# Kernel tuning notes

Measured on AMD Instinct MI355X. Metric: run time of the kernel, lower is better.

## Reference

```python
import jax, jax.numpy as jnp
import numpy as np

N = 50000        # nodes
E = 800000       # edges (before self-loops)
IN_C = 256
OUT_C = 64
HEADS = 4
NEG_SLOPE = 0.2  # PyG GATConv default


def setup_inputs() -> dict:
    key = jax.random.key(0)
    k0, k1, k2, k3, k4 = jax.random.split(key, 5)
    x = jax.random.normal(k0, (N, IN_C), jnp.float32)
    edge_index = jax.random.randint(k1, (2, E), 0, N, dtype=jnp.int32)
    W = jax.random.normal(k2, (IN_C, HEADS * OUT_C), jnp.float32) * (1.0 / np.sqrt(IN_C))
    att_src = jax.random.normal(k3, (HEADS, OUT_C), jnp.float32) * 0.1
    att_dst = jax.random.normal(k4, (HEADS, OUT_C), jnp.float32) * 0.1
    bias = jnp.zeros((OUT_C,), jnp.float32)
    return {"x": x, "edge_index": edge_index, "W": W,
            "att_src": att_src, "att_dst": att_dst, "bias": bias}


def reference(x, edge_index, W, att_src, att_dst, bias):
    n = x.shape[0]
    # PyG GATConv default add_self_loops=True
    loop = jnp.arange(n, dtype=edge_index.dtype)
    src = jnp.concatenate([edge_index[0], loop])  # [E+N]
    dst = jnp.concatenate([edge_index[1], loop])  # [E+N]

    h = (x @ W).reshape(n, HEADS, OUT_C)                    # [N,H,C]
    a_src = jnp.einsum('nhc,hc->nh', h, att_src)            # [N,H]
    a_dst = jnp.einsum('nhc,hc->nh', h, att_dst)            # [N,H]

    e = jax.nn.leaky_relu(a_src[src] + a_dst[dst], NEG_SLOPE)   # [E',H]
    # segment softmax over edges grouped by destination node
    m = jax.lax.stop_gradient(jax.ops.segment_max(e, dst, num_segments=n))  # [N,H]
    ex = jnp.exp(e - m[dst])
    denom = jax.ops.segment_sum(ex, dst, num_segments=n)    # [N,H]
    alpha = ex / (denom[dst] + 1e-16)                       # [E',H]

    out = jax.ops.segment_sum(alpha[:, :, None] * h[src], dst, num_segments=n)  # [N,H,C]
    # concat=False -> mean over heads, then bias
    return out.mean(axis=1) + bias
```

## Files before the change

### kernel.cpp

```cpp
#include <hip/hip_runtime.h>
#include <hip/hip_bf16.h>

#define INC   256
#define HEADS 4
#define OUTC  64
#define NEG_SLOPE 0.2f
#define CAP   5120
#define EPB_A 4096

typedef __attribute__((ext_vector_type(8))) short  fragA;
typedef __attribute__((ext_vector_type(4))) float  f32x4;

__device__ __forceinline__ float bf2f(unsigned short u) {
    union { unsigned int i; float f; } v; v.i = ((unsigned int)u) << 16; return v.f;
}
__device__ __forceinline__ unsigned short f2bf(float x) {
    __hip_bfloat16 b = __float2bfloat16(x);
    return *reinterpret_cast<unsigned short*>(&b);
}

__global__ __launch_bounds__(256) void wt_zero_kernel(const float* __restrict__ W,
                                                      unsigned short* __restrict__ Wt,
                                                      int* __restrict__ btail, int nbuck)
{
    int idx = blockIdx.x * 256 + threadIdx.x;
    int k = idx >> 8, c = idx & 255;
    Wt[c * 256 + k] = f2bf(W[k * 256 + c]);
    if (idx < nbuck) btail[idx] = 0;
}

__global__ __launch_bounds__(256, 2) void gemm_passA(
    const float* __restrict__ A,
    const unsigned short* __restrict__ Wt,
    const float* __restrict__ att_src,
    const float* __restrict__ att_dst,
    unsigned short* __restrict__ H2,
    float* __restrict__ a_srcO,
    float* __restrict__ a_dstO,
    int M,
    const int* __restrict__ src, const int* __restrict__ dst,
    int* __restrict__ btail,
    int2* __restrict__ bucketbuf,
    int E, int nbA)
{
    __shared__ __align__(16) unsigned short As[64 * 256];
    const int tid = threadIdx.x;

    if ((int)blockIdx.x < nbA) {
        char* sm = (char*)As;
        int* lhist = (int*)sm;
        int* lrankc = (int*)(sm + 1024);
        int* gbase  = (int*)(sm + 2048);
        lhist[tid] = 0; lrankc[tid] = 0;
        __syncthreads();
        int e0 = blockIdx.x * EPB_A;
        int e1 = e0 + EPB_A; if (e1 > E) e1 = E;
        for (int e = e0 + tid; e < e1; e += 256)
            atomicAdd(&lhist[dst[e] >> 8], 1);
        __syncthreads();
        {
            int c = lhist[tid];
            gbase[tid] = (c > 0) ? atomicAdd(&btail[tid], c) : 0;
        }
        __syncthreads();
        for (int e = e0 + tid; e < e1; e += 256) {
            int s = src[e], d = dst[e];
            int b = d >> 8;
            int r = atomicAdd(&lrankc[b], 1);
            bucketbuf[(size_t)b * CAP + gbase[b] + r] = make_int2(s, d);
        }
        return;
    }

    const int lane = tid & 63;
    const int wave = tid >> 6;
    const int row0 = ((int)blockIdx.x - nbA) * 64;
    const int g   = lane >> 4;
    const int r16 = lane & 15;

    fragA b[4][8];
    {
        const unsigned short* wp = Wt + (size_t)(wave * 64) * 256;
        #pragma unroll
        for (int nn = 0; nn < 4; ++nn)
            #pragma unroll
            for (int kk = 0; kk < 8; ++kk)
                b[nn][kk] = *(const fragA*)(wp + (size_t)(nn * 16 + r16) * 256 + kk * 32 + g * 8);
    }

    #pragma unroll
    for (int i = 0; i < 16; ++i) {
        int f   = i * 256 + tid;
        int row = f >> 6;
        int q   = f & 63;
        int gr  = row0 + row;
        float4 v = (gr < M) ? *(const float4*)(A + (size_t)gr * INC + q * 4)
                            : make_float4(0.f, 0.f, 0.f, 0.f);
        ushort4 u;
        u.x = f2bf(v.x); u.y = f2bf(v.y); u.z = f2bf(v.z); u.w = f2bf(v.w);
        int byte = (row << 9) + (q << 3);
        byte ^= (row & 7) << 4;
        *(ushort4*)((char*)As + byte) = u;
    }
    __syncthreads();

    f32x4 acc[4][4] = {};
    #pragma unroll
    for (int kk = 0; kk < 8; ++kk) {
        fragA a[4];
        #pragma unroll
        for (int m = 0; m < 4; ++m) {
            int row  = m * 16 + r16;
            int byte = (row << 9) + ((kk * 32 + g * 8) << 1);
            byte ^= (row & 7) << 4;
            a[m] = *(const fragA*)((const char*)As + byte);
        }
        #pragma unroll
        for (int m = 0; m < 4; ++m)
            #pragma unroll
            for (int nn = 0; nn < 4; ++nn)
                acc[m][nn] = __builtin_amdgcn_mfma_f32_16x16x32_bf16(
                    a[m], b[nn][kk], acc[m][nn], 0, 0, 0);
    }

    #pragma unroll
    for (int m = 0; m < 4; ++m) {
        #pragma unroll
        for (int nn = 0; nn < 4; ++nn) {
            int gcol = wave * 64 + nn * 16 + r16;
            #pragma unroll
            for (int r = 0; r < 4; ++r) {
                int grow = row0 + m * 16 + g * 4 + r;
                if (grow < M)
                    H2[(size_t)grow * (HEADS * OUTC) + gcol] = f2bf(acc[m][nn][r]);
            }
        }
    }

    {
        float as_att[4], ad_att[4];
        #pragma unroll
        for (int nn = 0; nn < 4; ++nn) {
            as_att[nn] = att_src[wave * 64 + nn * 16 + r16];
            ad_att[nn] = att_dst[wave * 64 + nn * 16 + r16];
        }
        float sv[4][4], dv[4][4];
        #pragma unroll
        for (int m = 0; m < 4; ++m)
            #pragma unroll
            for (int r = 0; r < 4; ++r) {
                float s = 0.f, d = 0.f;
                #pragma unroll
                for (int nn = 0; nn < 4; ++nn) {
                    s = fmaf(acc[m][nn][r], as_att[nn], s);
                    d = fmaf(acc[m][nn][r], ad_att[nn], d);
                }
                sv[m][r] = s; dv[m][r] = d;
            }
        #pragma unroll
        for (int off = 1; off < 16; off <<= 1) {
            #pragma unroll
            for (int m = 0; m < 4; ++m)
                #pragma unroll
                for (int r = 0; r < 4; ++r) {
                    sv[m][r] += __shfl_xor(sv[m][r], off, 64);
                    dv[m][r] += __shfl_xor(dv[m][r], off, 64);
                }
        }
        #pragma unroll
        for (int m = 0; m < 4; ++m)
            #pragma unroll
            for (int r = 0; r < 4; ++r) {
                if (r16 == m * 4 + r) {
                    int grow = row0 + m * 16 + g * 4 + r;
                    if (grow < M) {
                        a_srcO[(size_t)grow * HEADS + wave] = sv[m][r];
                        a_dstO[(size_t)grow * HEADS + wave] = dv[m][r];
                    }
                }
            }
    }
}

__global__ __launch_bounds__(256) void passB_kernel(const int2* __restrict__ bucketbuf,
                                                    const int* __restrict__ btail,
                                                    int* __restrict__ offsets,
                                                    int* __restrict__ esrc,
                                                    int N, int E)
{
    __shared__ int lcnt[256];
    __shared__ int red[256];
    __shared__ unsigned short lrank[CAP];
    const int b = blockIdx.x, t = threadIdx.x;

    int s0 = 0;
    for (int j = t; j < b; j += 256) s0 += btail[j];
    red[t] = s0;
    __syncthreads();
    for (int off = 128; off > 0; off >>= 1) {
        if (t < off) red[t] += red[t + off];
        __syncthreads();
    }
    const int baseg = red[0];
    const int cnt = btail[b];
    __syncthreads();

    lcnt[t] = 0;
    __syncthreads();
    const int2* bb = bucketbuf + (size_t)b * CAP;
    for (int i = t; i < cnt; i += 256)
        lrank[i] = (unsigned short)atomicAdd(&lcnt[bb[i].y & 255], 1);
    __syncthreads();

    int v = lcnt[t];
    red[t] = v;
    __syncthreads();
    for (int off = 1; off < 256; off <<= 1) {
        int x = (t >= off) ? red[t - off] : 0;
        __syncthreads();
        red[t] += x;
        __syncthreads();
    }
    int excl = red[t] - v;
    lcnt[t] = excl;
    int node = b * 256 + t;
    if (node < N) offsets[node] = baseg + excl;
    if (b == 0 && t == 0) offsets[N] = E;
    __syncthreads();

    for (int i = t; i < cnt; i += 256) {
        int2 sd = bb[i];
        int slot = baseg + lcnt[sd.y & 255] + lrank[i];
        esrc[slot] = sd.x;
    }
}

__global__ __launch_bounds__(128) void fused_agg_kernel(
    const unsigned short* __restrict__ h2,
    const float* __restrict__ a_src,
    const float* __restrict__ a_dst,
    const int*   __restrict__ offsets,
    const int*   __restrict__ esrc,
    const float* __restrict__ bias,
    float*       __restrict__ out,
    int n)
{
    int i    = (int)((blockIdx.x * blockDim.x + threadIdx.x) >> 6);
    int lane = threadIdx.x & 63;
    if (i >= n) return;
    const int h  = lane >> 4;
    const int cg = lane & 15;

    const float ad = a_dst[(size_t)i * HEADS + h];

    float acc0, acc1, acc2, acc3, l;
    {
        float as = a_src[(size_t)i * HEADS + h];
        float e = as + ad; e = e > 0.f ? e : NEG_SLOPE * e;
        float p = __expf(e);
        ushort4 v = *(const ushort4*)(h2 + (size_t)i * 256 + lane * 4);
        l = p;
        acc0 = p * bf2f(v.x);
        acc1 = p * bf2f(v.y);
        acc2 = p * bf2f(v.z);
        acc3 = p * bf2f(v.w);
    }

#define EDGE_BODY(S, AS)                                                     \
    {                                                                        \
        float e_ = (AS) + ad; e_ = e_ > 0.f ? e_ : NEG_SLOPE * e_;           \
        float p_ = __expf(e_);                                               \
        ushort4 v_ = *(const ushort4*)(h2 + (size_t)(S) * 256 + lane * 4);   \
        l += p_;                                                             \
        acc0 = fmaf(p_, bf2f(v_.x), acc0);                                   \
        acc1 = fmaf(p_, bf2f(v_.y), acc1);                                   \
        acc2 = fmaf(p_, bf2f(v_.z), acc2);                                   \
        acc3 = fmaf(p_, bf2f(v_.w), acc3);                                   \
    }

    int beg = offsets[i], end = offsets[i + 1];
    int j = beg;
    for (; j < end && (j & 3); ++j) {
        int s = esrc[j];
        float as = a_src[(size_t)s * HEADS + h];
        EDGE_BODY(s, as);
    }
    for (; j + 7 < end; j += 8) {
        int4 ea = *(const int4*)(esrc + j);
        int4 eb = *(const int4*)(esrc + j + 4);
        float as0 = a_src[(size_t)ea.x * HEADS + h];
        float as1 = a_src[(size_t)ea.y * HEADS + h];
        float as2 = a_src[(size_t)ea.z * HEADS + h];
        float as3 = a_src[(size_t)ea.w * HEADS + h];
        float as4 = a_src[(size_t)eb.x * HEADS + h];
        float as5 = a_src[(size_t)eb.y * HEADS + h];
        float as6 = a_src[(size_t)eb.z * HEADS + h];
        float as7 = a_src[(size_t)eb.w * HEADS + h];
        ushort4 v0 = *(const ushort4*)(h2 + (size_t)ea.x * 256 + lane * 4);
        ushort4 v1 = *(const ushort4*)(h2 + (size_t)ea.y * 256 + lane * 4);
        ushort4 v2 = *(const ushort4*)(h2 + (size_t)ea.z * 256 + lane * 4);
        ushort4 v3 = *(const ushort4*)(h2 + (size_t)ea.w * 256 + lane * 4);
        ushort4 v4 = *(const ushort4*)(h2 + (size_t)eb.x * 256 + lane * 4);
        ushort4 v5 = *(const ushort4*)(h2 + (size_t)eb.y * 256 + lane * 4);
        ushort4 v6 = *(const ushort4*)(h2 + (size_t)eb.z * 256 + lane * 4);
        ushort4 v7 = *(const ushort4*)(h2 + (size_t)eb.w * 256 + lane * 4);
        float e0 = as0 + ad; e0 = e0 > 0.f ? e0 : NEG_SLOPE * e0; float p0 = __expf(e0);
        float e1 = as1 + ad; e1 = e1 > 0.f ? e1 : NEG_SLOPE * e1; float p1 = __expf(e1);
        float e2 = as2 + ad; e2 = e2 > 0.f ? e2 : NEG_SLOPE * e2; float p2 = __expf(e2);
        float e3 = as3 + ad; e3 = e3 > 0.f ? e3 : NEG_SLOPE * e3; float p3 = __expf(e3);
        float e4 = as4 + ad; e4 = e4 > 0.f ? e4 : NEG_SLOPE * e4; float p4 = __expf(e4);
        float e5 = as5 + ad; e5 = e5 > 0.f ? e5 : NEG_SLOPE * e5; float p5 = __expf(e5);
        float e6 = as6 + ad; e6 = e6 > 0.f ? e6 : NEG_SLOPE * e6; float p6 = __expf(e6);
        float e7 = as7 + ad; e7 = e7 > 0.f ? e7 : NEG_SLOPE * e7; float p7 = __expf(e7);
        l += ((p0 + p1) + (p2 + p3)) + ((p4 + p5) + (p6 + p7));
        acc0 = fmaf(p0, bf2f(v0.x), acc0);
        acc1 = fmaf(p0, bf2f(v0.y), acc1);
        acc2 = fmaf(p0, bf2f(v0.z), acc2);
        acc3 = fmaf(p0, bf2f(v0.w), acc3);
        acc0 = fmaf(p1, bf2f(v1.x), acc0);
        acc1 = fmaf(p1, bf2f(v1.y), acc1);
        acc2 = fmaf(p1, bf2f(v1.z), acc2);
        acc3 = fmaf(p1, bf2f(v1.w), acc3);
        acc0 = fmaf(p2, bf2f(v2.x), acc0);
        acc1 = fmaf(p2, bf2f(v2.y), acc1);
        acc2 = fmaf(p2, bf2f(v2.z), acc2);
        acc3 = fmaf(p2, bf2f(v2.w), acc3);
        acc0 = fmaf(p3, bf2f(v3.x), acc0);
        acc1 = fmaf(p3, bf2f(v3.y), acc1);
        acc2 = fmaf(p3, bf2f(v3.z), acc2);
        acc3 = fmaf(p3, bf2f(v3.w), acc3);
        acc0 = fmaf(p4, bf2f(v4.x), acc0);
        acc1 = fmaf(p4, bf2f(v4.y), acc1);
        acc2 = fmaf(p4, bf2f(v4.z), acc2);
        acc3 = fmaf(p4, bf2f(v4.w), acc3);
        acc0 = fmaf(p5, bf2f(v5.x), acc0);
        acc1 = fmaf(p5, bf2f(v5.y), acc1);
        acc2 = fmaf(p5, bf2f(v5.z), acc2);
        acc3 = fmaf(p5, bf2f(v5.w), acc3);
        acc0 = fmaf(p6, bf2f(v6.x), acc0);
        acc1 = fmaf(p6, bf2f(v6.y), acc1);
        acc2 = fmaf(p6, bf2f(v6.z), acc2);
        acc3 = fmaf(p6, bf2f(v6.w), acc3);
        acc0 = fmaf(p7, bf2f(v7.x), acc0);
        acc1 = fmaf(p7, bf2f(v7.y), acc1);
        acc2 = fmaf(p7, bf2f(v7.z), acc2);
        acc3 = fmaf(p7, bf2f(v7.w), acc3);
    }
    if (j + 3 < end) {
        int4 ea = *(const int4*)(esrc + j);
        float as0 = a_src[(size_t)ea.x * HEADS + h];
        float as1 = a_src[(size_t)ea.y * HEADS + h];
        float as2 = a_src[(size_t)ea.z * HEADS + h];
        float as3 = a_src[(size_t)ea.w * HEADS + h];
        EDGE_BODY(ea.x, as0);
        EDGE_BODY(ea.y, as1);
        EDGE_BODY(ea.z, as2);
        EDGE_BODY(ea.w, as3);
        j += 4;
    }
    for (; j < end; ++j) {
        int s = esrc[j];
        float as = a_src[(size_t)s * HEADS + h];
        EDGE_BODY(s, as);
    }
#undef EDGE_BODY

    float inv = 1.f / (l + 1e-16f);
    float r0 = acc0 * inv, r1 = acc1 * inv, r2 = acc2 * inv, r3 = acc3 * inv;

    r0 += __shfl_xor(r0, 16, 64); r0 += __shfl_xor(r0, 32, 64);
    r1 += __shfl_xor(r1, 16, 64); r1 += __shfl_xor(r1, 32, 64);
    r2 += __shfl_xor(r2, 16, 64); r2 += __shfl_xor(r2, 32, 64);
    r3 += __shfl_xor(r3, 16, 64); r3 += __shfl_xor(r3, 32, 64);

    if (lane < 16) {
        float4 b4 = *(const float4*)(bias + cg * 4);
        float4 o;
        o.x = 0.25f * r0 + b4.x;
        o.y = 0.25f * r1 + b4.y;
        o.z = 0.25f * r2 + b4.z;
        o.w = 0.25f * r3 + b4.w;
        *(float4*)(out + (size_t)i * OUTC + cg * 4) = o;
    }
}

extern "C" void kernel_launch(void* const* d_in, const int* in_sizes, int n_in,
                              void* d_out, int out_size, void* d_ws, size_t ws_size,
                              hipStream_t stream)
{
    (void)n_in; (void)out_size; (void)ws_size;
    const float* x       = (const float*)d_in[0];
    const int*   edge    = (const int*)d_in[1];
    const float* W       = (const float*)d_in[2];
    const float* att_src = (const float*)d_in[3];
    const float* att_dst = (const float*)d_in[4];
    const float* bias    = (const float*)d_in[5];
    float* out = (float*)d_out;

    const int N = in_sizes[0] / INC;
    const int E = in_sizes[1] / 2;
    const int* srcA = edge;
    const int* dstA = edge + E;
    const int nbuck = (N + 255) / 256;
    const int nbA   = (E + EPB_A - 1) / EPB_A;

    char* ws = (char*)d_ws;
    unsigned short* h2 = (unsigned short*)ws; ws += (size_t)N * (HEADS * OUTC) * sizeof(unsigned short);
    unsigned short* Wt = (unsigned short*)ws; ws += (size_t)256 * 256 * sizeof(unsigned short);
    float* a_src  = (float*)ws; ws += (size_t)N * HEADS * sizeof(float);
    float* a_dst  = (float*)ws; ws += (size_t)N * HEADS * sizeof(float);
    int* offsets  = (int*)ws;   ws += (size_t)(N + 1) * sizeof(int) + 12;
    int* btail    = (int*)ws;   ws += (size_t)256 * sizeof(int);
    int2* bucketbuf = (int2*)ws; ws += (size_t)nbuck * CAP * sizeof(int2);
    int* esrc     = (int*)ws;   ws += (size_t)E * sizeof(int);

    wt_zero_kernel<<<256, 256, 0, stream>>>(W, Wt, btail, nbuck);

    gemm_passA<<<nbA + (N + 63) / 64, 256, 0, stream>>>(
        x, Wt, att_src, att_dst, h2, a_src, a_dst, N,
        srcA, dstA, btail, bucketbuf, E, nbA);

    passB_kernel<<<nbuck, 256, 0, stream>>>(bucketbuf, btail, offsets, esrc, N, E);

    fused_agg_kernel<<<(N + 1) / 2, 128, 0, stream>>>(h2, a_src, a_dst, offsets, esrc,
                                                      bias, out, N);
}
```

Measured before the change: 128.5 us.

## Sort nodes by in-degree so aggregation waves get balanced edge counts

Adds two small kernels that counting-sort the destination nodes by in-degree (capped at 63) into a permutation. The aggregation kernel then processes nodes in that order, so the two wavefronts in a block and neighbouring blocks see similar degrees and divergence and tail imbalance shrink. It also narrows the edge loop from 8 to 4 edges per iteration, which lowers register pressure but leaves fewer loads in flight. In exchange it adds two kernel launches and an extra level of indirection, and the output rows are written in a scattered order.

```diff
diff --git a/kernel.cpp b/kernel.cpp
--- a/kernel.cpp
+++ b/kernel.cpp
@@ -21,12 +21,14 @@
 
 __global__ __launch_bounds__(256) void wt_zero_kernel(const float* __restrict__ W,
                                                       unsigned short* __restrict__ Wt,
-                                                      int* __restrict__ btail, int nbuck)
+                                                      int* __restrict__ btail, int nbuck,
+                                                      int* __restrict__ dtotal)
 {
     int idx = blockIdx.x * 256 + threadIdx.x;
     int k = idx >> 8, c = idx & 255;
     Wt[c * 256 + k] = f2bf(W[k * 256 + c]);
     if (idx < nbuck) btail[idx] = 0;
+    if (idx < 64)    dtotal[idx] = 0;
 }
 
 __global__ __launch_bounds__(256, 2) void gemm_passA(
@@ -235,30 +237,77 @@
     }
 }
 
+__global__ __launch_bounds__(256) void dsort1_kernel(const int* __restrict__ offsets,
+                                                     int* __restrict__ dtotal,
+                                                     int* __restrict__ blockbase,
+                                                     int N)
+{
+    __shared__ int lh[64];
+    const int t = threadIdx.x, b = blockIdx.x;
+    const int i = b * 256 + t;
+    if (t < 64) lh[t] = 0;
+    __syncthreads();
+    if (i < N) {
+        int deg = offsets[i + 1] - offsets[i];
+        if (deg > 63) deg = 63;
+        atomicAdd(&lh[deg], 1);
+    }
+    __syncthreads();
+    if (t < 64) blockbase[b * 64 + t] = atomicAdd(&dtotal[t], lh[t]);
+}
+
+__global__ __launch_bounds__(256) void dsort2_kernel(const int* __restrict__ offsets,
+                                                     const int* __restrict__ dtotal,
+                                                     const int* __restrict__ blockbase,
+                                                     int* __restrict__ perm,
+                                                     int N)
+{
+    __shared__ int lr[64], dbase[64];
+    const int t = threadIdx.x, b = blockIdx.x;
+    const int i = b * 256 + t;
+    if (t < 64) { lr[t] = 0; dbase[t] = dtotal[t]; }
+    __syncthreads();
+    if (t == 0) {
+        int run = 0;
+        #pragma unroll 1
+        for (int d = 0; d < 64; ++d) { int c = dbase[d]; dbase[d] = run; run += c; }
+    }
+    __syncthreads();
+    if (i < N) {
+        int deg = offsets[i + 1] - offsets[i];
+        if (deg > 63) deg = 63;
+        int r = atomicAdd(&lr[deg], 1);
+        perm[dbase[deg] + blockbase[b * 64 + deg] + r] = i;
+    }
+}
+
 __global__ __launch_bounds__(128) void fused_agg_kernel(
     const unsigned short* __restrict__ h2,
     const float* __restrict__ a_src,
     const float* __restrict__ a_dst,
     const int*   __restrict__ offsets,
     const int*   __restrict__ esrc,
+    const int*   __restrict__ perm,
     const float* __restrict__ bias,
     float*       __restrict__ out,
     int n)
 {
-    int i    = (int)((blockIdx.x * blockDim.x + threadIdx.x) >> 6);
+    int w    = (int)((blockIdx.x * blockDim.x + threadIdx.x) >> 6);
     int lane = threadIdx.x & 63;
-    if (i >= n) return;
+    if (w >= n) return;
+    const int i  = perm[w];
     const int h  = lane >> 4;
     const int cg = lane & 15;
 
     const float ad = a_dst[(size_t)i * HEADS + h];
+    const unsigned short* h2p = h2 + lane * 4;
 
     float acc0, acc1, acc2, acc3, l;
     {
         float as = a_src[(size_t)i * HEADS + h];
         float e = as + ad; e = e > 0.f ? e : NEG_SLOPE * e;
         float p = __expf(e);
-        ushort4 v = *(const ushort4*)(h2 + (size_t)i * 256 + lane * 4);
+        ushort4 v = *(const ushort4*)(h2p + (size_t)i * 256);
         l = p;
         acc0 = p * bf2f(v.x);
         acc1 = p * bf2f(v.y);
@@ -270,7 +319,7 @@
     {                                                                        \
         float e_ = (AS) + ad; e_ = e_ > 0.f ? e_ : NEG_SLOPE * e_;           \
         float p_ = __expf(e_);                                               \
-        ushort4 v_ = *(const ushort4*)(h2 + (size_t)(S) * 256 + lane * 4);   \
+        ushort4 v_ = *(const ushort4*)(h2p + (size_t)(S) * 256);             \
         l += p_;                                                             \
         acc0 = fmaf(p_, bf2f(v_.x), acc0);                                   \
         acc1 = fmaf(p_, bf2f(v_.y), acc1);                                   \
@@ -285,34 +334,21 @@
         float as = a_src[(size_t)s * HEADS + h];
         EDGE_BODY(s, as);
     }
-    for (; j + 7 < end; j += 8) {
+    for (; j + 3 < end; j += 4) {
         int4 ea = *(const int4*)(esrc + j);
-        int4 eb = *(const int4*)(esrc + j + 4);
         float as0 = a_src[(size_t)ea.x * HEADS + h];
         float as1 = a_src[(size_t)ea.y * HEADS + h];
         float as2 = a_src[(size_t)ea.z * HEADS + h];
         float as3 = a_src[(size_t)ea.w * HEADS + h];
-        float as4 = a_src[(size_t)eb.x * HEADS + h];
-        float as5 = a_src[(size_t)eb.y * HEADS + h];
-        float as6 = a_src[(size_t)eb.z * HEADS + h];
-        float as7 = a_src[(size_t)eb.w * HEADS + h];
-        ushort4 v0 = *(const ushort4*)(h2 + (size_t)ea.x * 256 + lane * 4);
-        ushort4 v1 = *(const ushort4*)(h2 + (size_t)ea.y * 256 + lane * 4);
-        ushort4 v2 = *(const ushort4*)(h2 + (size_t)ea.z * 256 + lane * 4);
-        ushort4 v3 = *(const ushort4*)(h2 + (size_t)ea.w * 256 + lane * 4);
-        ushort4 v4 = *(const ushort4*)(h2 + (size_t)eb.x * 256 + lane * 4);
-        ushort4 v5 = *(const ushort4*)(h2 + (size_t)eb.y * 256 + lane * 4);
-        ushort4 v6 = *(const ushort4*)(h2 + (size_t)eb.z * 256 + lane * 4);
-        ushort4 v7 = *(const ushort4*)(h2 + (size_t)eb.w * 256 + lane * 4);
+        ushort4 v0 = *(const ushort4*)(h2p + (size_t)ea.x * 256);
+        ushort4 v1 = *(const ushort4*)(h2p + (size_t)ea.y * 256);
+        ushort4 v2 = *(const ushort4*)(h2p + (size_t)ea.z * 256);
+        ushort4 v3 = *(const ushort4*)(h2p + (size_t)ea.w * 256);
         float e0 = as0 + ad; e0 = e0 > 0.f ? e0 : NEG_SLOPE * e0; float p0 = __expf(e0);
         float e1 = as1 + ad; e1 = e1 > 0.f ? e1 : NEG_SLOPE * e1; float p1 = __expf(e1);
         float e2 = as2 + ad; e2 = e2 > 0.f ? e2 : NEG_SLOPE * e2; float p2 = __expf(e2);
         float e3 = as3 + ad; e3 = e3 > 0.f ? e3 : NEG_SLOPE * e3; float p3 = __expf(e3);
-        float e4 = as4 + ad; e4 = e4 > 0.f ? e4 : NEG_SLOPE * e4; float p4 = __expf(e4);
-        float e5 = as5 + ad; e5 = e5 > 0.f ? e5 : NEG_SLOPE * e5; float p5 = __expf(e5);
-        float e6 = as6 + ad; e6 = e6 > 0.f ? e6 : NEG_SLOPE * e6; float p6 = __expf(e6);
-        float e7 = as7 + ad; e7 = e7 > 0.f ? e7 : NEG_SLOPE * e7; float p7 = __expf(e7);
-        l += ((p0 + p1) + (p2 + p3)) + ((p4 + p5) + (p6 + p7));
+        l += (p0 + p1) + (p2 + p3);
         acc0 = fmaf(p0, bf2f(v0.x), acc0);
         acc1 = fmaf(p0, bf2f(v0.y), acc1);
         acc2 = fmaf(p0, bf2f(v0.z), acc2);
@@ -329,34 +365,6 @@
         acc1 = fmaf(p3, bf2f(v3.y), acc1);
         acc2 = fmaf(p3, bf2f(v3.z), acc2);
         acc3 = fmaf(p3, bf2f(v3.w), acc3);
-        acc0 = fmaf(p4, bf2f(v4.x), acc0);
-        acc1 = fmaf(p4, bf2f(v4.y), acc1);
-        acc2 = fmaf(p4, bf2f(v4.z), acc2);
-        acc3 = fmaf(p4, bf2f(v4.w), acc3);
-        acc0 = fmaf(p5, bf2f(v5.x), acc0);
-        acc1 = fmaf(p5, bf2f(v5.y), acc1);
-        acc2 = fmaf(p5, bf2f(v5.z), acc2);
-        acc3 = fmaf(p5, bf2f(v5.w), acc3);
-        acc0 = fmaf(p6, bf2f(v6.x), acc0);
-        acc1 = fmaf(p6, bf2f(v6.y), acc1);
-        acc2 = fmaf(p6, bf2f(v6.z), acc2);
-        acc3 = fmaf(p6, bf2f(v6.w), acc3);
-        acc0 = fmaf(p7, bf2f(v7.x), acc0);
-        acc1 = fmaf(p7, bf2f(v7.y), acc1);
-        acc2 = fmaf(p7, bf2f(v7.z), acc2);
-        acc3 = fmaf(p7, bf2f(v7.w), acc3);
-    }
-    if (j + 3 < end) {
-        int4 ea = *(const int4*)(esrc + j);
-        float as0 = a_src[(size_t)ea.x * HEADS + h];
-        float as1 = a_src[(size_t)ea.y * HEADS + h];
-        float as2 = a_src[(size_t)ea.z * HEADS + h];
-        float as3 = a_src[(size_t)ea.w * HEADS + h];
-        EDGE_BODY(ea.x, as0);
-        EDGE_BODY(ea.y, as1);
-        EDGE_BODY(ea.z, as2);
-        EDGE_BODY(ea.w, as3);
-        j += 4;
     }
     for (; j < end; ++j) {
         int s = esrc[j];
@@ -403,6 +411,7 @@
     const int* dstA = edge + E;
     const int nbuck = (N + 255) / 256;
     const int nbA   = (E + EPB_A - 1) / EPB_A;
+    const int nbn   = (N + 255) / 256;
 
     char* ws = (char*)d_ws;
     unsigned short* h2 = (unsigned short*)ws; ws += (size_t)N * (HEADS * OUTC) * sizeof(unsigned short);
@@ -411,10 +420,13 @@
     float* a_dst  = (float*)ws; ws += (size_t)N * HEADS * sizeof(float);
     int* offsets  = (int*)ws;   ws += (size_t)(N + 1) * sizeof(int) + 12;
     int* btail    = (int*)ws;   ws += (size_t)256 * sizeof(int);
+    int* dtotal   = (int*)ws;   ws += (size_t)64 * sizeof(int);
+    int* blockbase= (int*)ws;   ws += (size_t)nbn * 64 * sizeof(int);
+    int* perm     = (int*)ws;   ws += (size_t)N * sizeof(int);
     int2* bucketbuf = (int2*)ws; ws += (size_t)nbuck * CAP * sizeof(int2);
     int* esrc     = (int*)ws;   ws += (size_t)E * sizeof(int);
 
-    wt_zero_kernel<<<256, 256, 0, stream>>>(W, Wt, btail, nbuck);
+    wt_zero_kernel<<<256, 256, 0, stream>>>(W, Wt, btail, nbuck, dtotal);
 
     gemm_passA<<<nbA + (N + 63) / 64, 256, 0, stream>>>(
         x, Wt, att_src, att_dst, h2, a_src, a_dst, N,
@@ -422,6 +434,9 @@
 
     passB_kernel<<<nbuck, 256, 0, stream>>>(bucketbuf, btail, offsets, esrc, N, E);
 
+    dsort1_kernel<<<nbn, 256, 0, stream>>>(offsets, dtotal, blockbase, N);
+    dsort2_kernel<<<nbn, 256, 0, stream>>>(offsets, dtotal, blockbase, perm, N);
+
     fused_agg_kernel<<<(N + 1) / 2, 128, 0, stream>>>(h2, a_src, a_dst, offsets, esrc,
-                                                      bias, out, N);
-}
+                                                      perm, bias, out, N);
+}
```

Result: slower. 140.7 us (+9.5%).
